# Kernel optimization log

Measured on AMD Instinct MI355X. Metric: run time of the kernel, lower is better.

Reference implementation:

```python
import jax, jax.numpy as jnp
import numpy as np

# Module constants (globals in the original source)
N_SPECIAL = 5            # len(SPECIAL_TOKENS)
LABEL_ID = 2             # SPECIAL_TOKENS['<LABEL>']
ACT_VOCAB = 64           # ACTIVITY_VOCAB_SIZE
TIME_VOCAB = 32          # TIME_BUCKET_VOCAB_SIZE
VOCAB = N_SPECIAL + ACT_VOCAB + TIME_VOCAB  # 101


def setup_inputs() -> dict:
    key = jax.random.key(0)
    ks = jax.random.split(key, 8)
    B, T, D = 8, 2048, 1024
    tokens = jax.random.randint(ks[0], (B, T), 0, VOCAB)
    h = jax.random.normal(ks[1], (B, T, D), dtype=jnp.float32)
    E = jax.random.normal(ks[2], (VOCAB, D), dtype=jnp.float32) * 0.02
    W_next = jax.random.normal(ks[3], (ACT_VOCAB, D), dtype=jnp.float32) * (1.0 / np.sqrt(D))
    b_next = jnp.zeros((ACT_VOCAB,), jnp.float32)
    W_time = jax.random.normal(ks[4], (TIME_VOCAB, D), dtype=jnp.float32) * (1.0 / np.sqrt(D))
    b_time = jnp.zeros((TIME_VOCAB,), jnp.float32)
    return {
        'tokens': tokens, 'h': h, 'E': E,
        'W_next': W_next, 'b_next': b_next,
        'W_time': W_time, 'b_time': b_time,
        'tied_scale_act': jnp.asarray(0.0, jnp.float32),
        'tied_scale_time': jnp.asarray(0.0, jnp.float32),
        'copy_scale_act': jnp.asarray(1.5, jnp.float32),
        'copy_scale_time': jnp.asarray(1.5, jnp.float32),
        'copy_temp_act': jnp.asarray(1.0, jnp.float32),
        'copy_temp_time': jnp.asarray(1.0, jnp.float32),
    }


def _heads(tokens, h, E, W_next, b_next, W_time, b_time,
           tied_scale_act, tied_scale_time, copy_scale_act, copy_scale_time,
           copy_temp_act, copy_temp_time):
    act_start = N_SPECIAL
    time_start = N_SPECIAL + ACT_VOCAB
    sp = jax.nn.softplus

    # Parametric heads: [B,T,A], [B,T,Tb]
    param_next = jnp.einsum('btd,ad->bta', h, W_next) + b_next
    param_time = jnp.einsum('btd,cd->btc', h, W_time) + b_time

    # Weight-tied heads from slices of the token-embedding table
    tied_act = jnp.einsum('btd,ad->bta', h, E[act_start:act_start + ACT_VOCAB])
    tied_time = jnp.einsum('btd,cd->btc', h, E[time_start:time_start + TIME_VOCAB])

    # --- Retrieval/copy head, fully vectorized over (b, query, key) ---
    # F.normalize(h, dim=-1) with eps clamp
    hn = h / jnp.maximum(jnp.linalg.norm(h, axis=-1, keepdims=True), 1e-12)
    sims = jnp.einsum('bqd,bkd->bqk', hn, hn)  # [B,T,T] cosine sims

    T = tokens.shape[1]
    is_label = tokens == LABEL_ID                           # [B,T] query gate
    value_mask = jnp.pad(is_label[:, :-1], ((0, 0), (1, 0)))  # pos whose prev tok is <LABEL>
    val_act = value_mask & (tokens >= act_start) & (tokens < time_start)
    val_time = value_mask & (tokens >= time_start) & (tokens < time_start + TIME_VOCAB)
    strict_past = jnp.tril(jnp.ones((T, T), bool), -1)      # key k < query q

    def copy_logits(val_mask, class_idx, n_cls, tau):
        m = is_label[:, :, None] & strict_past[None] & val_mask[:, None, :]
        s = jnp.where(m, sims, 0.0) * tau                   # masked, scaled sims
        onehot = jax.nn.one_hot(jnp.clip(class_idx, 0, n_cls - 1), n_cls, dtype=h.dtype)
        # segment-sum into class buckets: [B,q,k] @ [B,k,c] -> [B,q,c]
        return jnp.einsum('bqk,bkc->bqc', s, onehot)

    copy_act = copy_logits(val_act, tokens - act_start, ACT_VOCAB, sp(copy_temp_act))
    copy_time = copy_logits(val_time, tokens - time_start, TIME_VOCAB, sp(copy_temp_time))

    activity_logits = param_next + sp(tied_scale_act) * tied_act + sp(copy_scale_act) * copy_act
    time_logits = param_time + sp(tied_scale_time) * tied_time + sp(copy_scale_time) * copy_time
    return activity_logits, time_logits


def reference(tokens, h, E, W_next, b_next, W_time, b_time,
              tied_scale_act, tied_scale_time, copy_scale_act, copy_scale_time,
              copy_temp_act, copy_temp_time):
    return _heads(tokens, h, E, W_next, b_next, W_time, b_time,
                  tied_scale_act, tied_scale_time, copy_scale_act, copy_scale_time,
                  copy_temp_act, copy_temp_time)
```

## Files before the change

### kernel.cpp

```cpp
#include <hip/hip_runtime.h>
#include <hip/hip_bf16.h>

#define BATCH  8
#define T_TOK  2048
#define DMODEL 1024
#define BT     (BATCH * T_TOK)
#define NCOLS  96
#define KSPLIT 4

typedef __bf16 bf16x8 __attribute__((ext_vector_type(8)));
typedef float  f32x4  __attribute__((ext_vector_type(4)));
typedef unsigned short u16x8 __attribute__((ext_vector_type(8)));

union AB { u16x8 u; bf16x8 b; unsigned int w[4]; };

__device__ __forceinline__ unsigned short f2bf(float f) {
    unsigned u = __float_as_uint(f);
    unsigned r = (u + 0x7fffu + ((u >> 16) & 1u)) >> 16;
    return (unsigned short)r;
}
__device__ __forceinline__ float softplusf(float x) {
    return fmaxf(x, 0.f) + log1pf(expf(-fabsf(x)));
}
__device__ __forceinline__ float wave_sum(float v) {
#pragma unroll
    for (int o = 32; o > 0; o >>= 1) v += __shfl_xor(v, o, 64);
    return v;
}
__device__ __forceinline__ unsigned int pack_rtz(float lo, float hi) {
    return __builtin_amdgcn_perm(__float_as_uint(hi), __float_as_uint(lo), 0x07060302u);
}
__device__ __forceinline__ void atomic_fadd(float* p, float v) {
    unsafeAtomicAdd(p, v);
}

__global__ __launch_bounds__(256) void prep_init_kernel(
    const float* __restrict__ E,
    const float* __restrict__ Wn,
    const float* __restrict__ bn,
    const float* __restrict__ Wt,
    const float* __restrict__ bt,
    const float* __restrict__ tsa,
    const float* __restrict__ tst,
    unsigned short* __restrict__ Weff,
    float* __restrict__ out)
{
    const int blk = blockIdx.x;
    if (blk < 384) {
        int idx = blk * 256 + threadIdx.x;
        int row = idx >> 10, k = idx & 1023;
        float w;
        if (row < 64) {
            w = Wn[idx] + softplusf(tsa[0]) * E[(5 + row) * 1024 + k];
        } else {
            int c = row - 64;
            w = Wt[c * 1024 + k] + softplusf(tst[0]) * E[(69 + c) * 1024 + k];
        }
        Weff[idx] = f2bf(w);
    } else {
        int i = (blk - 384) * 256 + threadIdx.x;
        if (i < 262144) {
            float4 b = reinterpret_cast<const float4*>(bn)[i & 15];
            reinterpret_cast<float4*>(out)[i] = b;
        } else {
            int k = i - 262144;
            float4 b = reinterpret_cast<const float4*>(bt)[k & 7];
            reinterpret_cast<float4*>(out)[i] = b;
        }
    }
}

__global__ __launch_bounds__(256) void gemm_kernel(
    const float* __restrict__ h,
    const unsigned short* __restrict__ Weff,
    float* __restrict__ out)
{
    const int lane = threadIdx.x & 63;
    const int wave = threadIdx.x >> 6;
    const int m = lane & 15;
    const int q = lane >> 4;
    const int tok_base = (blockIdx.x * 4 + wave) * 16;
    const int kbase = blockIdx.y * 32;

    const float4* hA = reinterpret_cast<const float4*>(h + (size_t)(tok_base + m) * DMODEL);
    const bf16x8* wB = reinterpret_cast<const bf16x8*>(Weff + (size_t)m * DMODEL);

    f32x4 acc[6];
#pragma unroll
    for (int n = 0; n < 6; ++n) acc[n] = (f32x4){0.f, 0.f, 0.f, 0.f};

#pragma unroll
    for (int kc = 0; kc < 32; kc += 4) {
        const int ch = kbase + kc + q;
        float4 f0 = hA[ch * 2];
        float4 f1 = hA[ch * 2 + 1];
        AB a;
        a.w[0] = pack_rtz(f0.x, f0.y);
        a.w[1] = pack_rtz(f0.z, f0.w);
        a.w[2] = pack_rtz(f1.x, f1.y);
        a.w[3] = pack_rtz(f1.z, f1.w);
#pragma unroll
        for (int n = 0; n < 6; ++n) {
            acc[n] = __builtin_amdgcn_mfma_f32_16x16x32_bf16(a.b, wB[n * 2048 + ch], acc[n], 0, 0, 0);
        }
    }

#pragma unroll
    for (int n = 0; n < 6; ++n) {
        const int j = n * 16 + m;
#pragma unroll
        for (int r = 0; r < 4; ++r) {
            const int t = tok_base + q * 4 + r;
            float* dst = (j < 64) ? &out[(size_t)t * 64 + j]
                                  : &out[(size_t)BT * 64 + (size_t)t * 32 + (j - 64)];
            atomic_fadd(dst, acc[n][r]);
        }
    }
}

__global__ __launch_bounds__(1024) void copy_kernel(
    const int* __restrict__ tokens,
    const float* __restrict__ h,
    const float* __restrict__ csa,
    const float* __restrict__ cst,
    const float* __restrict__ cta,
    const float* __restrict__ ctt,
    float* __restrict__ out)
{
    const int b     = blockIdx.x >> 3;
    const int slice = blockIdx.x & 7;
    const int tid  = threadIdx.x;
    const int wave = tid >> 6, lane = tid & 63;

    __shared__ int cnt_q[32], cnt_k[32], off_q[32], off_k[32];
    __shared__ int s_nq, s_nk;
    __shared__ int   q_pos[T_TOK];
    __shared__ int   k_pos[T_TOK];
    __shared__ int   k_col[T_TOK];
    __shared__ float q_nrm[T_TOK];
    __shared__ float k_nrm[T_TOK];

    const int* tk = tokens + b * T_TOK;

#pragma unroll
    for (int c = 0; c < 2; ++c) {
        int chunk = wave * 2 + c;
        int t = chunk * 64 + lane;
        int v = tk[t];
        bool pq = (v == 2);
        bool pk = (t > 0) && (tk[t - 1] == 2) && (v >= 5) && (v < 101);
        unsigned long long mq = __ballot(pq);
        unsigned long long mk = __ballot(pk);
        if (lane == 0) { cnt_q[chunk] = __popcll(mq); cnt_k[chunk] = __popcll(mk); }
    }
    __syncthreads();
    if (tid == 0) {
        int aq = 0, ak = 0;
        for (int i = 0; i < 32; ++i) {
            off_q[i] = aq; aq += cnt_q[i];
            off_k[i] = ak; ak += cnt_k[i];
        }
        s_nq = aq; s_nk = ak;
    }
    __syncthreads();

#pragma unroll
    for (int c = 0; c < 2; ++c) {
        int chunk = wave * 2 + c;
        int t = chunk * 64 + lane;
        int v = tk[t];
        bool pq = (v == 2);
        bool pk = (t > 0) && (tk[t - 1] == 2) && (v >= 5) && (v < 101);
        unsigned long long mq = __ballot(pq);
        unsigned long long mk = __ballot(pk);
        unsigned long long below = (lane == 0) ? 0ull : ((~0ull) >> (64 - lane));
        if (pq) q_pos[off_q[chunk] + __popcll(mq & below)] = t;
        if (pk) {
            int i = off_k[chunk] + __popcll(mk & below);
            k_pos[i] = t;
            k_col[i] = (v < 69) ? (v - 5) : (64 + (v - 69));
        }
    }
    __syncthreads();
    const int nq = s_nq, nk = s_nk;
    const float* hb = h + (size_t)b * T_TOK * DMODEL;

    for (int i = wave; i < nq + nk; i += 16) {
        const int row = (i < nq) ? q_pos[i] : k_pos[i - nq];
        const float4* p = reinterpret_cast<const float4*>(hb + (size_t)row * DMODEL);
        float s = 0.f;
#pragma unroll
        for (int c = 0; c < 4; ++c) {
            float4 v = p[lane + c * 64];
            s += v.x * v.x + v.y * v.y + v.z * v.z + v.w * v.w;
        }
        s = wave_sum(s);
        if (lane == 0) {
            float nn = fmaxf(sqrtf(s), 1e-12f);
            if (i < nq) q_nrm[i] = nn; else k_nrm[i - nq] = nn;
        }
    }
    __syncthreads();

    const float fa = softplusf(csa[0]) * softplusf(cta[0]);
    const float ft = softplusf(cst[0]) * softplusf(ctt[0]);
    const int P = nq * nk;
    const int g = slice * 16 + wave;
    for (int p = g; p < P; p += 128) {
        const int qi = p / nk, ki = p - qi * nk;
        const int qp = q_pos[qi], kp = k_pos[ki];
        if (kp >= qp) continue;
        const float4* pq = reinterpret_cast<const float4*>(hb + (size_t)qp * DMODEL);
        const float4* pk = reinterpret_cast<const float4*>(hb + (size_t)kp * DMODEL);
        float s = 0.f;
#pragma unroll
        for (int c = 0; c < 4; ++c) {
            float4 va = pq[lane + c * 64];
            float4 vb = pk[lane + c * 64];
            s += va.x * vb.x + va.y * vb.y + va.z * vb.z + va.w * vb.w;
        }
        s = wave_sum(s);
        if (lane == 0) {
            const int col = k_col[ki];
            const float val = ((col < 64) ? fa : ft) * (s / (q_nrm[qi] * k_nrm[ki]));
            const size_t tg = (size_t)b * T_TOK + qp;
            float* dst = (col < 64) ? &out[tg * 64 + col]
                                    : &out[(size_t)BT * 64 + tg * 32 + (col - 64)];
            atomic_fadd(dst, val);
        }
    }
}

extern "C" void kernel_launch(void* const* d_in, const int* in_sizes, int n_in,
                              void* d_out, int out_size, void* d_ws, size_t ws_size,
                              hipStream_t stream) {
    const int* tokens = (const int*)d_in[0];
    const float* h    = (const float*)d_in[1];
    const float* E    = (const float*)d_in[2];
    const float* Wn   = (const float*)d_in[3];
    const float* bn   = (const float*)d_in[4];
    const float* Wt   = (const float*)d_in[5];
    const float* bt   = (const float*)d_in[6];
    const float* tsa  = (const float*)d_in[7];
    const float* tst  = (const float*)d_in[8];
    const float* csa  = (const float*)d_in[9];
    const float* cst  = (const float*)d_in[10];
    const float* cta  = (const float*)d_in[11];
    const float* ctt  = (const float*)d_in[12];

    unsigned short* Weff = (unsigned short*)d_ws;
    float* out           = (float*)d_out;

    prep_init_kernel<<<dim3(1920), dim3(256), 0, stream>>>(E, Wn, bn, Wt, bt, tsa, tst, Weff, out);
    gemm_kernel<<<dim3(BT / 64, KSPLIT), dim3(256), 0, stream>>>(h, Weff, out);
    copy_kernel<<<dim3(64), dim3(1024), 0, stream>>>(tokens, h, csa, cst, cta, ctt, out);
}
```

Measured before the change: 167.4 us.

## Stage fused head weights in swizzled LDS via async loads, prefetch h into registers

The GEMM kernel now copies each block's 96x256 bf16 weight slice into shared memory with global_load_lds async copies, using an XOR swizzle to avoid bank conflicts. The four waves then read B fragments from LDS instead of each reading them from global memory. All of a wave's h inputs for its K-quarter are loaded into registers before the MFMA loop, so memory latency is exposed once up front. This costs 48KB of LDS per block and more registers, and launch bounds are set to 3 blocks per CU. The copy kernel only has a variable renamed.

```diff
diff --git a/kernel.cpp b/kernel.cpp
--- a/kernel.cpp
+++ b/kernel.cpp
@@ -7,6 +7,7 @@
 #define BT     (BATCH * T_TOK)
 #define NCOLS  96
 #define KSPLIT 4
+#define KQ     256
 
 typedef __bf16 bf16x8 __attribute__((ext_vector_type(8)));
 typedef float  f32x4  __attribute__((ext_vector_type(4)));
@@ -32,6 +33,11 @@
 }
 __device__ __forceinline__ void atomic_fadd(float* p, float v) {
     unsafeAtomicAdd(p, v);
+}
+__device__ __forceinline__ void async16(const void* g, void* l) {
+    __builtin_amdgcn_global_load_lds(
+        (const __attribute__((address_space(1))) unsigned int*)g,
+        (__attribute__((address_space(3))) unsigned int*)l, 16, 0, 0);
 }
 
 __global__ __launch_bounds__(256) void prep_init_kernel(
@@ -70,38 +76,59 @@
     }
 }
 
-__global__ __launch_bounds__(256) void gemm_kernel(
+__global__ __launch_bounds__(256, 3) void gemm_kernel(
     const float* __restrict__ h,
     const unsigned short* __restrict__ Weff,
     float* __restrict__ out)
 {
-    const int lane = threadIdx.x & 63;
-    const int wave = threadIdx.x >> 6;
+    __shared__ float4 Bbuf[3072];
+
+    const int tid  = threadIdx.x;
+    const int lane = tid & 63;
+    const int wave = tid >> 6;
     const int m = lane & 15;
     const int q = lane >> 4;
-    const int tok_base = (blockIdx.x * 4 + wave) * 16;
-    const int kbase = blockIdx.y * 32;
-
-    const float4* hA = reinterpret_cast<const float4*>(h + (size_t)(tok_base + m) * DMODEL);
-    const bf16x8* wB = reinterpret_cast<const bf16x8*>(Weff + (size_t)m * DMODEL);
+    const int tok0 = blockIdx.x * 64;
+    const int kq   = blockIdx.y;
+
+    const float* hrow = h + (size_t)(tok0 + wave * 16 + m) * DMODEL + kq * KQ;
+    float4 areg[16];
+#pragma unroll
+    for (int kw = 0; kw < 8; ++kw) {
+        areg[kw * 2]     = *reinterpret_cast<const float4*>(hrow + kw * 32 + q * 8);
+        areg[kw * 2 + 1] = *reinterpret_cast<const float4*>(hrow + kw * 32 + q * 8 + 4);
+    }
+
+#pragma unroll
+    for (int i = 0; i < 12; ++i) {
+        int u = i * 256 + tid;
+        int row = u >> 5, c = u & 31;
+        async16(Weff + (size_t)row * DMODEL + kq * KQ + ((c ^ (row & 7)) << 3),
+                &Bbuf[u]);
+    }
+    __syncthreads();
 
     f32x4 acc[6];
 #pragma unroll
     for (int n = 0; n < 6; ++n) acc[n] = (f32x4){0.f, 0.f, 0.f, 0.f};
 
-#pragma unroll
-    for (int kc = 0; kc < 32; kc += 4) {
-        const int ch = kbase + kc + q;
-        float4 f0 = hA[ch * 2];
-        float4 f1 = hA[ch * 2 + 1];
+    const int s = m & 7;
+#pragma unroll
+    for (int kw = 0; kw < 8; ++kw) {
+        float4 f0 = areg[kw * 2];
+        float4 f1 = areg[kw * 2 + 1];
         AB a;
         a.w[0] = pack_rtz(f0.x, f0.y);
         a.w[1] = pack_rtz(f0.z, f0.w);
         a.w[2] = pack_rtz(f1.x, f1.y);
         a.w[3] = pack_rtz(f1.z, f1.w);
+        const int cu = kw * 4 + q;
 #pragma unroll
         for (int n = 0; n < 6; ++n) {
-            acc[n] = __builtin_amdgcn_mfma_f32_16x16x32_bf16(a.b, wB[n * 2048 + ch], acc[n], 0, 0, 0);
+            const int rb = n * 16 + m;
+            const bf16x8* bp = reinterpret_cast<const bf16x8*>(
+                &Bbuf[rb * 32 + (cu ^ s)]);
+            acc[n] = __builtin_amdgcn_mfma_f32_16x16x32_bf16(a.b, *bp, acc[n], 0, 0, 0);
         }
     }
 
@@ -109,11 +136,11 @@
     for (int n = 0; n < 6; ++n) {
         const int j = n * 16 + m;
 #pragma unroll
-        for (int r = 0; r < 4; ++r) {
-            const int t = tok_base + q * 4 + r;
+        for (int rr = 0; rr < 4; ++rr) {
+            const int t = tok0 + wave * 16 + q * 4 + rr;
             float* dst = (j < 64) ? &out[(size_t)t * 64 + j]
                                   : &out[(size_t)BT * 64 + (size_t)t * 32 + (j - 64)];
-            atomic_fadd(dst, acc[n][r]);
+            atomic_fadd(dst, acc[n][rr]);
         }
     }
 }
@@ -188,15 +215,15 @@
     for (int i = wave; i < nq + nk; i += 16) {
         const int row = (i < nq) ? q_pos[i] : k_pos[i - nq];
         const float4* p = reinterpret_cast<const float4*>(hb + (size_t)row * DMODEL);
-        float s = 0.f;
+        float ssum = 0.f;
 #pragma unroll
         for (int c = 0; c < 4; ++c) {
             float4 v = p[lane + c * 64];
-            s += v.x * v.x + v.y * v.y + v.z * v.z + v.w * v.w;
-        }
-        s = wave_sum(s);
+            ssum += v.x * v.x + v.y * v.y + v.z * v.z + v.w * v.w;
+        }
+        ssum = wave_sum(ssum);
         if (lane == 0) {
-            float nn = fmaxf(sqrtf(s), 1e-12f);
+            float nn = fmaxf(sqrtf(ssum), 1e-12f);
             if (i < nq) q_nrm[i] = nn; else k_nrm[i - nq] = nn;
         }
     }
@@ -212,17 +239,17 @@
         if (kp >= qp) continue;
         const float4* pq = reinterpret_cast<const float4*>(hb + (size_t)qp * DMODEL);
         const float4* pk = reinterpret_cast<const float4*>(hb + (size_t)kp * DMODEL);
-        float s = 0.f;
+        float ssum = 0.f;
 #pragma unroll
         for (int c = 0; c < 4; ++c) {
             float4 va = pq[lane + c * 64];
             float4 vb = pk[lane + c * 64];
-            s += va.x * vb.x + va.y * vb.y + va.z * vb.z + va.w * vb.w;
-        }
-        s = wave_sum(s);
+            ssum += va.x * vb.x + va.y * vb.y + va.z * vb.z + va.w * vb.w;
+        }
+        ssum = wave_sum(ssum);
         if (lane == 0) {
             const int col = k_col[ki];
-            const float val = ((col < 64) ? fa : ft) * (s / (q_nrm[qi] * k_nrm[ki]));
+            const float val = ((col < 64) ? fa : ft) * (ssum / (q_nrm[qi] * k_nrm[ki]));
             const size_t tg = (size_t)b * T_TOK + qp;
             float* dst = (col < 64) ? &out[tg * 64 + col]
                                     : &out[(size_t)BT * 64 + tg * 32 + (col - 64)];
```

New measurement: 147.7 us. -11.8%, faster.
